# Kernel optimization log

Measured on AMD Instinct MI355X. Metric: run time of the kernel, lower is better.

Reference implementation:

```python
import jax, jax.numpy as jnp
import numpy as np

N, IND, B = 1_000_000, 64, 100  # rows, input features, num_grid (outd = B+1)


def setup_inputs() -> dict:
    key = jax.random.key(0)
    k1, k2, k3, k4 = jax.random.split(key, 4)
    return {
        "t": jax.random.uniform(k1, (N,), dtype=jnp.float32),          # bounded in [0,1]
        "x": jax.random.normal(k2, (N, IND), dtype=jnp.float32),
        "weight": jax.random.uniform(k3, (IND, B + 1), dtype=jnp.float32),  # torch.rand init
        "bias": jax.random.uniform(k4, (B + 1,), dtype=jnp.float32),
        "num_grid": B,
    }


def reference(t, x, weight, bias, num_grid):
    # linear + bias + softmax over bins
    out = x @ weight + bias                      # [N, B+1]
    out1 = jax.nn.softmax(out, axis=1)           # [N, B+1]
    # comp_grid: data-dependent bin indices with linear interpolation weight
    tB = t * num_grid
    U = jnp.ceil(tB)                             # upper bin (float)
    inter = 1.0 - (U - tB)                       # interpolation weight toward U
    L = U - 1.0
    L = jnp.where(L < 0, L + 1.0, L)             # L += (L < 0)
    Li = L.astype(jnp.int32)
    Ui = U.astype(jnp.int32)
    # per-row dual gather + lerp
    L_out = jnp.take_along_axis(out1, Li[:, None], axis=1)[:, 0]  # [N]
    U_out = jnp.take_along_axis(out1, Ui[:, None], axis=1)[:, 0]  # [N]
    out_interp = L_out + (U_out - L_out) * inter
    return (out1, out_interp)
```

## Files before the change

kernel.cpp:

```cpp
#include <hip/hip_runtime.h>
#include <math.h>

#define IND   64
#define OUTD  101
#define RPB   64
#define NCT   7
#define LROW  101
#define QTR_WORDS (16 * OUTD)

typedef _Float16 half8 __attribute__((ext_vector_type(8)));
typedef float    f32x4 __attribute__((ext_vector_type(4)));

__global__ __launch_bounds__(64, 3) void density_kernel(
    const float* __restrict__ t,
    const float* __restrict__ x,
    const float* __restrict__ weight,
    const float* __restrict__ bias,
    const int*   __restrict__ num_grid,
    float* __restrict__ out1,
    float* __restrict__ out_interp,
    int n_rows, int n_tiles, int n_blocks)
{
    __shared__ float ptile[QTR_WORDS];

    const int lane = threadIdx.x;
    const int lc   = lane & 15;
    const int lg   = lane >> 4;
    const float ngf = (float)num_grid[0];

    half8 wf[NCT][2];
    float biasv[NCT];
#pragma unroll
    for (int ct = 0; ct < NCT; ++ct) {
        const int col  = ct * 16 + lc;
        const int colc = (col < OUTD) ? col : (OUTD - 1);
        biasv[ct] = (col < OUTD) ? bias[col] : -1e30f;
#pragma unroll
        for (int kg = 0; kg < 2; ++kg) {
            half8 h;
#pragma unroll
            for (int j = 0; j < 8; ++j)
                h[j] = (_Float16)weight[(kg * 32 + lg * 8 + j) * OUTD + colc];
            wf[ct][kg] = h;
        }
    }

    #define XPTR(TILE, RT) \
        ((const f32x4*)(x + (size_t)min((TILE) * RPB + (RT) * 16 + lc, n_rows - 1) * IND + lg * 8))

    f32x4 pa0, pa1, pa2, pa3, pb0, pb1, pb2, pb3;

    int tile = blockIdx.x;
    {
        const f32x4* p = XPTR(tile, 0);
        pa0 = p[0]; pa1 = p[1]; pa2 = p[8]; pa3 = p[9];
    }

    #define PROCESS(RT, C0, C1, C2, C3, N0, N1, N2, N3, PT, PR)                  \
    {                                                                            \
        {   const f32x4* np = XPTR(PT, PR);                                      \
            N0 = np[0]; N1 = np[1]; N2 = np[8]; N3 = np[9]; }                    \
        half8 a0, a1;                                                            \
        _Pragma("unroll")                                                        \
        for (int i = 0; i < 4; ++i) {                                            \
            a0[i] = (_Float16)C0[i]; a0[4 + i] = (_Float16)C1[i];                \
            a1[i] = (_Float16)C2[i]; a1[4 + i] = (_Float16)C3[i];                \
        }                                                                        \
        f32x4 c[NCT];                                                            \
        _Pragma("unroll")                                                        \
        for (int ct = 0; ct < NCT; ++ct) {                                       \
            f32x4 ci = {biasv[ct], biasv[ct], biasv[ct], biasv[ct]};             \
            ci = __builtin_amdgcn_mfma_f32_16x16x32_f16(a0, wf[ct][0], ci,0,0,0);\
            ci = __builtin_amdgcn_mfma_f32_16x16x32_f16(a1, wf[ct][1], ci,0,0,0);\
            c[ct] = ci;                                                          \
        }                                                                        \
        float m[4], s[4];                                                        \
        _Pragma("unroll")                                                        \
        for (int j = 0; j < 4; ++j) {                                            \
            float mj = c[0][j];                                                  \
            _Pragma("unroll")                                                    \
            for (int ct = 1; ct < NCT; ++ct) mj = fmaxf(mj, c[ct][j]);           \
            _Pragma("unroll")                                                    \
            for (int d = 1; d < 16; d <<= 1) mj = fmaxf(mj, __shfl_xor(mj,d,64));\
            m[j] = mj; s[j] = 0.0f;                                              \
        }                                                                        \
        _Pragma("unroll")                                                        \
        for (int ct = 0; ct < NCT; ++ct)                                         \
            _Pragma("unroll")                                                    \
            for (int j = 0; j < 4; ++j) {                                        \
                const float e = __expf(c[ct][j] - m[j]);                         \
                c[ct][j] = e; s[j] += e;                                         \
            }                                                                    \
        _Pragma("unroll")                                                        \
        for (int j = 0; j < 4; ++j) {                                            \
            _Pragma("unroll")                                                    \
            for (int d = 1; d < 16; d <<= 1) s[j] += __shfl_xor(s[j], d, 64);    \
            float inv = __builtin_amdgcn_rcpf(s[j]);                             \
            inv = inv * (2.0f - s[j] * inv);                                     \
            s[j] = inv;                                                          \
        }                                                                        \
        _Pragma("unroll")                                                        \
        for (int ct = 0; ct < NCT; ++ct) {                                       \
            const int col = ct * 16 + lc;                                        \
            if (col < OUTD) {                                                    \
                _Pragma("unroll")                                                \
                for (int j = 0; j < 4; ++j)                                      \
                    ptile[(lg * 4 + j) * LROW + col] = c[ct][j] * s[j];          \
            }                                                                    \
        }                                                                        \
    }

    #define DRAIN(Q)                                                             \
    {                                                                            \
        float* obase = out1 + (size_t)tile * (RPB * OUTD) + (Q) * QTR_WORDS;     \
        if (row0 + RPB <= n_rows) {                                              \
            _Pragma("unroll")                                                    \
            for (int i = 0; i < 6; ++i) {                                        \
                const f32x4 v = *(const f32x4*)&ptile[i * 256 + lane * 4];       \
                __builtin_nontemporal_store(v, (f32x4*)(obase + i * 256 + lane * 4)); \
            }                                                                    \
            if (lane < 20) {                                                     \
                const f32x4 v = *(const f32x4*)&ptile[1536 + lane * 4];          \
                __builtin_nontemporal_store(v, (f32x4*)(obase + 1536 + lane * 4)); \
            }                                                                    \
        } else {          \
            for (int r = 0; r < 16; ++r) {                                       \
                const int grr = row0 + (Q) * 16 + r;                             \
                if (grr < n_rows)                                                \
                    for (int cc = lane; cc < OUTD; cc += 64)                     \
                        out1[(size_t)grr * OUTD + cc] = ptile[r * LROW + cc];    \
            }                                                                    \
        }                                                                        \
                \
        if ((lane >> 4) == (Q) && gr < n_rows) {                                 \
            const float Lv = ptile[(lane & 15) * LROW + Li];                     \
            const float Uv = ptile[(lane & 15) * LROW + Ui];                     \
            out_interp[gr] = Lv + (Uv - Lv) * inter;                             \
        }                                                                        \
    }

    for (; tile < n_tiles; tile += n_blocks) {
        const int row0 = tile * RPB;

        const int gr  = row0 + lane;
        const int grc = (gr < n_rows) ? gr : (n_rows - 1);
        const float tB = t[grc] * ngf;
        const float Uf = ceilf(tB);
        const float inter = 1.0f - (Uf - tB);
        float Lf = Uf - 1.0f;
        if (Lf < 0.0f) Lf += 1.0f;
        const int Li = (int)Lf, Ui = (int)Uf;

        const int  ntile = tile + n_blocks;
        const int  pt    = (ntile < n_tiles) ? ntile : tile;

        PROCESS(0, pa0, pa1, pa2, pa3, pb0, pb1, pb2, pb3, tile, 1)
        DRAIN(0)
        PROCESS(1, pb0, pb1, pb2, pb3, pa0, pa1, pa2, pa3, tile, 2)
        DRAIN(1)
        PROCESS(2, pa0, pa1, pa2, pa3, pb0, pb1, pb2, pb3, tile, 3)
        DRAIN(2)
        PROCESS(3, pb0, pb1, pb2, pb3, pa0, pa1, pa2, pa3, pt,   0)
        DRAIN(3)
    }
    #undef DRAIN
    #undef PROCESS
    #undef XPTR
}

extern "C" void kernel_launch(void* const* d_in, const int* in_sizes, int n_in,
                              void* d_out, int out_size, void* d_ws, size_t ws_size,
                              hipStream_t stream) {
    const float* t  = (const float*)d_in[0];
    const float* x  = (const float*)d_in[1];
    const float* w  = (const float*)d_in[2];
    const float* b  = (const float*)d_in[3];
    const int*   ng = (const int*)d_in[4];
    const int n_rows = in_sizes[0];

    float* out1       = (float*)d_out;
    float* out_interp = out1 + (size_t)n_rows * OUTD;

    const int n_tiles  = (n_rows + RPB - 1) / RPB;
    const int n_blocks = 4096;
    density_kernel<<<dim3(n_blocks), dim3(64), 0, stream>>>(
        t, x, w, b, ng, out1, out_interp, n_rows, n_tiles, n_blocks);
}
```

Measured before the change: 128.1 us.

## Launch one block per tile instead of persistent grid-stride blocks

Replaces the persistent 4096-block grid-stride loop with a launch of one 64-thread block per 64-row tile (about 15.6k blocks), removing cross-tile prefetch of x. The intent is to rely on hardware scheduling and more blocks in flight to hide memory latency instead of software prefetch across tiles. In exchange, each block now reloads the weight fragments and bias from global memory and converts them to half precision. The last quarter also no longer prefetches the next tile.

Result: slower. 142.8 us (+11.5%).

```diff
diff --git a/kernel.cpp b/kernel.cpp
--- a/kernel.cpp
+++ b/kernel.cpp
@@ -19,7 +19,7 @@
     const int*   __restrict__ num_grid,
     float* __restrict__ out1,
     float* __restrict__ out_interp,
-    int n_rows, int n_tiles, int n_blocks)
+    int n_rows)
 {
     __shared__ float ptile[QTR_WORDS];
 
@@ -27,6 +27,8 @@
     const int lc   = lane & 15;
     const int lg   = lane >> 4;
     const float ngf = (float)num_grid[0];
+    const int tile = blockIdx.x;
+    const int row0 = tile * RPB;
 
     half8 wf[NCT][2];
     float biasv[NCT];
@@ -45,21 +47,16 @@
         }
     }
 
-    #define XPTR(TILE, RT) \
-        ((const f32x4*)(x + (size_t)min((TILE) * RPB + (RT) * 16 + lc, n_rows - 1) * IND + lg * 8))
+    #define XPTR(RT) \
+        ((const f32x4*)(x + (size_t)min(row0 + (RT) * 16 + lc, n_rows - 1) * IND + lg * 8))
 
     f32x4 pa0, pa1, pa2, pa3, pb0, pb1, pb2, pb3;
-
-    int tile = blockIdx.x;
     {
-        const f32x4* p = XPTR(tile, 0);
+        const f32x4* p = XPTR(0);
         pa0 = p[0]; pa1 = p[1]; pa2 = p[8]; pa3 = p[9];
     }
 
-    #define PROCESS(RT, C0, C1, C2, C3, N0, N1, N2, N3, PT, PR)                  \
-    {                                                                            \
-        {   const f32x4* np = XPTR(PT, PR);                                      \
-            N0 = np[0]; N1 = np[1]; N2 = np[8]; N3 = np[9]; }                    \
+    #define BODY(C0, C1, C2, C3)                                                 \
         half8 a0, a1;                                                            \
         _Pragma("unroll")                                                        \
         for (int i = 0; i < 4; ++i) {                                            \
@@ -107,7 +104,17 @@
                 for (int j = 0; j < 4; ++j)                                      \
                     ptile[(lg * 4 + j) * LROW + col] = c[ct][j] * s[j];          \
             }                                                                    \
-        }                                                                        \
+        }
+
+    #define PROCESS(C0, C1, C2, C3, N0, N1, N2, N3, PR)                          \
+    {                                                                            \
+        {   const f32x4* np = XPTR(PR);                                          \
+            N0 = np[0]; N1 = np[1]; N2 = np[8]; N3 = np[9]; }                    \
+        BODY(C0, C1, C2, C3)                                                     \
+    }
+    #define PROCESS_NOPF(C0, C1, C2, C3)                                         \
+    {                                                                            \
+        BODY(C0, C1, C2, C3)                                                     \
     }
 
     #define DRAIN(Q)                                                             \
@@ -139,32 +146,28 @@
         }                                                                        \
     }
 
-    for (; tile < n_tiles; tile += n_blocks) {
-        const int row0 = tile * RPB;
+    const int gr  = row0 + lane;
+    const int grc = (gr < n_rows) ? gr : (n_rows - 1);
+    const float tB = t[grc] * ngf;
+    const float Uf = ceilf(tB);
+    const float inter = 1.0f - (Uf - tB);
+    float Lf = Uf - 1.0f;
+    if (Lf < 0.0f) Lf += 1.0f;
+    const int Li = (int)Lf, Ui = (int)Uf;
 
-        const int gr  = row0 + lane;
-        const int grc = (gr < n_rows) ? gr : (n_rows - 1);
-        const float tB = t[grc] * ngf;
-        const float Uf = ceilf(tB);
-        const float inter = 1.0f - (Uf - tB);
-        float Lf = Uf - 1.0f;
-        if (Lf < 0.0f) Lf += 1.0f;
-        const int Li = (int)Lf, Ui = (int)Uf;
+    PROCESS(pa0, pa1, pa2, pa3, pb0, pb1, pb2, pb3, 1)
+    DRAIN(0)
+    PROCESS(pb0, pb1, pb2, pb3, pa0, pa1, pa2, pa3, 2)
+    DRAIN(1)
+    PROCESS(pa0, pa1, pa2, pa3, pb0, pb1, pb2, pb3, 3)
+    DRAIN(2)
+    PROCESS_NOPF(pb0, pb1, pb2, pb3)
+    DRAIN(3)
 
-        const int  ntile = tile + n_blocks;
-        const int  pt    = (ntile < n_tiles) ? ntile : tile;
-
-        PROCESS(0, pa0, pa1, pa2, pa3, pb0, pb1, pb2, pb3, tile, 1)
-        DRAIN(0)
-        PROCESS(1, pb0, pb1, pb2, pb3, pa0, pa1, pa2, pa3, tile, 2)
-        DRAIN(1)
-        PROCESS(2, pa0, pa1, pa2, pa3, pb0, pb1, pb2, pb3, tile, 3)
-        DRAIN(2)
-        PROCESS(3, pb0, pb1, pb2, pb3, pa0, pa1, pa2, pa3, pt,   0)
-        DRAIN(3)
-    }
     #undef DRAIN
     #undef PROCESS
+    #undef PROCESS_NOPF
+    #undef BODY
     #undef XPTR
 }
 
@@ -181,8 +184,7 @@
     float* out1       = (float*)d_out;
     float* out_interp = out1 + (size_t)n_rows * OUTD;
 
-    const int n_tiles  = (n_rows + RPB - 1) / RPB;
-    const int n_blocks = 4096;
+    const int n_blocks = (n_rows + RPB - 1) / RPB;
     density_kernel<<<dim3(n_blocks), dim3(64), 0, stream>>>(
-        t, x, w, b, ng, out1, out_interp, n_rows, n_tiles, n_blocks);
+        t, x, w, b, ng, out1, out_interp, n_rows);
 }
```
